# Optimization experiments

Measured on AMD Instinct MI355X. Metric: run time of the kernel, lower is better.

The kernel has to match this reference:

```python
import jax, jax.numpy as jnp
import numpy as np

N_NODES = 100000
N_EDGES = 1600000
D_IN = 128
D_OUT = 128


def setup_inputs() -> dict:
    key = jax.random.key(0)
    k_x, k_e, k_wl, k_bl, k_wr = jax.random.split(key, 5)
    x = jax.random.normal(k_x, (N_NODES, D_IN), dtype=jnp.float32)
    edge_index = jax.random.randint(k_e, (2, N_EDGES), 0, N_NODES, dtype=jnp.int64)
    # PyG Linear default init ~ kaiming-uniform-ish; plain uniform is fine for a numeric reference
    s = 1.0 / np.sqrt(D_IN)
    W_l = jax.random.uniform(k_wl, (D_OUT, D_IN), minval=-s, maxval=s, dtype=jnp.float32)
    b_l = jax.random.uniform(k_bl, (D_OUT,), minval=-s, maxval=s, dtype=jnp.float32)
    W_r = jax.random.uniform(k_wr, (D_OUT, D_IN), minval=-s, maxval=s, dtype=jnp.float32)
    return {"x": x, "edge_index": edge_index, "W_l": W_l, "b_l": b_l, "W_r": W_r}


def reference(x, edge_index, W_l, b_l, W_r):
    # SAGEConv (mean aggr): messages flow src -> dst
    src = edge_index[0]  # [E]
    dst = edge_index[1]  # [E]
    msgs = x[src]  # [E, D_IN] neighbor gather
    summed = jax.ops.segment_sum(msgs, dst, num_segments=N_NODES)  # [N, D_IN]
    deg = jax.ops.segment_sum(jnp.ones_like(dst, dtype=x.dtype), dst, num_segments=N_NODES)  # [N]
    agg = summed / jnp.maximum(deg, 1.0)[:, None]  # mean with 0 for isolated nodes
    # out = lin_l(agg) + lin_r(x); bias only on lin_l (PyG default)
    out = agg @ W_l.T + b_l + x @ W_r.T
    return out
```

## Files before the change

### kernel.cpp

```cpp
#include <hip/hip_runtime.h>

#define D_FEAT 128
#define CAP 32
#define S1CAP (1 << 16)
#define S2CAP (1 << 16)
#define LOGB 7
#define LOCB 128
#define BCAP 2560
#define CHUNK 8192
#define NBUK_MAX 1024
#define BPAD 8

typedef short bf16x8 __attribute__((ext_vector_type(8)));
typedef float f32x4 __attribute__((ext_vector_type(4)));

__device__ __forceinline__ unsigned short f2bf(float f) {
    unsigned u = __builtin_bit_cast(unsigned, f);
    u += 0x7FFF + ((u >> 16) & 1);
    return (unsigned short)(u >> 16);
}


__global__ __launch_bounds__(256) void tprep_kernel(
    const int* __restrict__ ei, int* __restrict__ flag, int* __restrict__ s1cnt,
    int* __restrict__ s2cnt, int* __restrict__ bincnt) {
    const int b = blockIdx.x;
    const int t = threadIdx.x;
    for (int i = b * 256 + t; i < NBUK_MAX * BPAD; i += 8 * 256) bincnt[i] = 0;
    if (b == 0) {
        __shared__ int nzs[4];
        int nz = 0;
        for (int i = t; i < 4096; i += 256) nz |= (ei[2 * i + 1] != 0);
        unsigned long long bal = __ballot(nz);
        if ((t & 63) == 0) nzs[t >> 6] = (bal != 0ull) ? 1 : 0;
        __syncthreads();
        if (t == 0) {
            *flag = (nzs[0] | nzs[1] | nzs[2] | nzs[3]) ? 0 : 1;
            *s1cnt = 0;
            *s2cnt = 0;
        }
    }
}

__global__ __launch_bounds__(256) void bwx_kernel(
    const int* __restrict__ ei, const int* __restrict__ flag,
    int* __restrict__ bincnt, unsigned* __restrict__ bins,
    int* __restrict__ s1cnt, int* __restrict__ spill1, int E, int N, int NBUK,
    int BINB,
    const float* __restrict__ Wl, const float* __restrict__ Wr,
    unsigned short* __restrict__ Wc,
    const float4* __restrict__ x4, uint2* __restrict__ xb2, long total4) {
    const int b = blockIdx.x;
    const int t = threadIdx.x;

    if (b < BINB) {
        __shared__ int hist[NBUK_MAX];
        __shared__ int rbase[NBUK_MAX];
        const long e0 = (long)b * CHUNK;
        const int cnt = (int)min((long)CHUNK, (long)E - e0);
        const int is64 = *flag;

        for (int i = t; i < NBUK; i += 256) hist[i] = 0;
        __syncthreads();

        for (int i = t; i < cnt; i += 256) {
            long e = e0 + i;
            int dst = is64 ? (int)((const long long*)ei)[(long)E + e] : ei[(long)E + e];
            dst = min(max(dst, 0), N - 1);
            atomicAdd(&hist[dst >> LOGB], 1);
        }
        __syncthreads();

        for (int i = t; i < NBUK; i += 256) {
            int h = hist[i];
            rbase[i] = (h > 0) ? atomicAdd(&bincnt[i * BPAD], h) : 0;
            hist[i] = 0;
        }
        __syncthreads();

        for (int i = t; i < cnt; i += 256) {
            long e = e0 + i;
            int src, dst;
            if (is64) {
                src = (int)((const long long*)ei)[e];
                dst = (int)((const long long*)ei)[(long)E + e];
            } else {
                src = ei[e];
                dst = ei[(long)E + e];
            }
            src = min(max(src, 0), N - 1);
            dst = min(max(dst, 0), N - 1);
            int bk = dst >> LOGB;
            int slot = rbase[bk] + atomicAdd(&hist[bk], 1);
            if (slot < BCAP) {
                bins[(long)bk * BCAP + slot] =
                    ((unsigned)(dst & (LOCB - 1)) << 25) | (unsigned)src;
            } else {
                int sp = atomicAdd(s1cnt, 1);
                if (sp < S1CAP) {
                    spill1[2 * sp] = src;
                    spill1[2 * sp + 1] = dst;
                }
            }
        }
    } else if (b < BINB + 128) {
        int n = b - BINB;
        float w = (t < 128) ? Wl[n * 128 + t] : Wr[n * 128 + (t - 128)];
        Wc[n * 256 + t] = f2bf(w);
    } else {
        long gid = (long)(b - BINB - 128) * 256 + t;
        if (gid < total4) {
            float4 v = x4[gid];
            uint2 o;
            o.x = (unsigned)f2bf(v.x) | ((unsigned)f2bf(v.y) << 16);
            o.y = (unsigned)f2bf(v.z) | ((unsigned)f2bf(v.w) << 16);
            xb2[gid] = o;
        }
    }
}

__global__ __launch_bounds__(256) void fill2_kernel(
    const unsigned* __restrict__ bins, const int* __restrict__ bincnt,
    int* __restrict__ adj, int* __restrict__ cursor,
    const int* __restrict__ s1cnt, const int* __restrict__ spill1,
    int* __restrict__ s2cnt, int* __restrict__ spill2, int N) {
    __shared__ int cur[LOCB];
    const int bk = blockIdx.x;
    const int t = threadIdx.x;
    if (t < LOCB) cur[t] = 0;
    __syncthreads();
    const int cnt = min(bincnt[bk * BPAD], BCAP);
    const int nb = bk << LOGB;
    for (int i = t; i < cnt; i += 256) {
        unsigned v = bins[(long)bk * BCAP + i];
        int src = (int)(v & 0x1FFFFFFu);
        int ld = (int)(v >> 25);
        int slot = atomicAdd(&cur[ld], 1);
        int dst = nb + ld;
        if (slot < CAP) {
            adj[(long)dst * CAP + slot] = src;
        } else {
            int sp = atomicAdd(s2cnt, 1);
            if (sp < S2CAP) {
                spill2[2 * sp] = src;
                spill2[2 * sp + 1] = dst;
            }
        }
    }
    const int sc = min(*s1cnt, S1CAP);
    for (int i = t; i < sc; i += 256) {
        int dst = spill1[2 * i + 1];
        if ((dst >> LOGB) == bk) {
            int src = spill1[2 * i];
            int ld = dst & (LOCB - 1);
            int slot = atomicAdd(&cur[ld], 1);
            if (slot < CAP) {
                adj[(long)dst * CAP + slot] = src;
            } else {
                int sp = atomicAdd(s2cnt, 1);
                if (sp < S2CAP) {
                    spill2[2 * sp] = src;
                    spill2[2 * sp + 1] = dst;
                }
            }
        }
    }
    __syncthreads();
    if (t < LOCB && nb + t < N) cursor[nb + t] = cur[t];
}

__device__ __forceinline__ void acc_row(float* acc, uint4 v) {
    acc[0] += __builtin_bit_cast(float, v.x << 16);
    acc[1] += __builtin_bit_cast(float, v.x & 0xFFFF0000u);
    acc[2] += __builtin_bit_cast(float, v.y << 16);
    acc[3] += __builtin_bit_cast(float, v.y & 0xFFFF0000u);
    acc[4] += __builtin_bit_cast(float, v.z << 16);
    acc[5] += __builtin_bit_cast(float, v.z & 0xFFFF0000u);
    acc[6] += __builtin_bit_cast(float, v.w << 16);
    acc[7] += __builtin_bit_cast(float, v.w & 0xFFFF0000u);
}

__device__ __forceinline__ int pick_src(int adjv, int adjv2, int e, int cq, int qd) {
    int ec = e & 31;
    int s = __shfl((ec < 16) ? adjv : adjv2, qd * 16 + (ec & 15));
    return (e < cq) ? s : 0;
}

__global__ __launch_bounds__(256) void gg_kernel(
    const unsigned int* __restrict__ xb, const int* __restrict__ cursor,
    const int* __restrict__ adj, const unsigned short* __restrict__ Wc,
    const float* __restrict__ bl, float* __restrict__ out, int N) {
    __shared__ __align__(16) unsigned short A[16 * 264];

    const int t = threadIdx.x;
    const int wv = t >> 6;
    const int lane = t & 63;
    const int n0 = blockIdx.x * 16;
    const int fq = lane & 15;
    const int qd = lane >> 4;

    const int n = n0 + wv * 4 + qd;
    const int nc = min(n, N - 1);

    const int deg = (n < N) ? cursor[n] : 0;
    int adjv = adj[(long)nc * CAP + fq];
    int adjv2 = adj[(long)nc * CAP + 16 + fq];

    unsigned xv[4];
#pragma unroll
    for (int q = 0; q < 4; ++q) {
        int nn = n0 + wv * 4 + q;
        xv[q] = (nn < N) ? xb[(long)nn * 64 + lane] : 0u;
    }

    adjv = min(max(adjv, 0), N - 1);
    adjv2 = min(max(adjv2, 0), N - 1);

    const int cq = min(deg, CAP);
    int mx = max(cq, __shfl_xor(cq, 16));
    mx = max(mx, __shfl_xor(mx, 32));
    mx = (mx + 3) & ~3;

    float acc[8] = {0.f, 0.f, 0.f, 0.f, 0.f, 0.f, 0.f, 0.f};
    uint4 va[4], vb[4];
#pragma unroll
    for (int j = 0; j < 4; ++j) {
        int s = pick_src(adjv, adjv2, j, cq, qd);
        va[j] = *(const uint4*)&xb[(long)s * 64 + fq * 4];
    }
    for (int base = 0; base < mx; base += 4) {
#pragma unroll
        for (int j = 0; j < 4; ++j) {
            int s = pick_src(adjv, adjv2, base + 4 + j, cq, qd);
            vb[j] = *(const uint4*)&xb[(long)s * 64 + fq * 4];
        }
#pragma unroll
        for (int j = 0; j < 4; ++j) {
            if (base + j < cq) acc_row(acc, va[j]);
        }
#pragma unroll
        for (int j = 0; j < 4; ++j) va[j] = vb[j];
    }

    const float iv = 1.0f / (float)max(deg, 1);
    uint4 o;
    o.x = (unsigned)f2bf(acc[0] * iv) | ((unsigned)f2bf(acc[1] * iv) << 16);
    o.y = (unsigned)f2bf(acc[2] * iv) | ((unsigned)f2bf(acc[3] * iv) << 16);
    o.z = (unsigned)f2bf(acc[4] * iv) | ((unsigned)f2bf(acc[5] * iv) << 16);
    o.w = (unsigned)f2bf(acc[6] * iv) | ((unsigned)f2bf(acc[7] * iv) << 16);
    *(uint4*)&A[(wv * 4 + qd) * 264 + fq * 8] = o;
#pragma unroll
    for (int q = 0; q < 4; ++q)
        *(unsigned*)&A[(wv * 4 + q) * 264 + 128 + 2 * lane] = xv[q];
    __syncthreads();

    const int l15 = lane & 15;
    const int quad = lane >> 4;
    f32x4 acc2[2];
    acc2[0] = (f32x4){0.f, 0.f, 0.f, 0.f};
    acc2[1] = (f32x4){0.f, 0.f, 0.f, 0.f};

#pragma unroll
    for (int kc = 0; kc < 8; ++kc) {
        const int k0 = kc * 32;
        bf16x8 af = *(const bf16x8*)&A[l15 * 264 + k0 + quad * 8];
#pragma unroll
        for (int nt = 0; nt < 2; ++nt) {
            int col = wv * 32 + nt * 16 + l15;
            bf16x8 bf = *(const bf16x8*)&Wc[col * 256 + k0 + quad * 8];
            acc2[nt] = __builtin_amdgcn_mfma_f32_16x16x32_bf16(af, bf, acc2[nt], 0, 0, 0);
        }
    }

#pragma unroll
    for (int nt = 0; nt < 2; ++nt) {
        int col = wv * 32 + nt * 16 + l15;
        float bias = bl[col];
#pragma unroll
        for (int r = 0; r < 4; ++r) {
            int node = n0 + quad * 4 + r;
            if (node < N) out[(long)node * 128 + col] = acc2[nt][r] + bias;
        }
    }
}

__global__ __launch_bounds__(256) void spill2_kernel(
    const float* __restrict__ x, const float* __restrict__ Wl,
    const int* __restrict__ cursor, const int* __restrict__ s2cnt,
    const int* __restrict__ spill2, float* __restrict__ out) {
    const int wv = threadIdx.x >> 6;
    const int lane = threadIdx.x & 63;
    const int sc = min(*s2cnt, S2CAP);
    for (int i = blockIdx.x * 4 + wv; i < sc; i += gridDim.x * 4) {
        int src = spill2[2 * i];
        int dst = spill2[2 * i + 1];
        float inv = 1.0f / (float)max(cursor[dst], 1);
#pragma unroll
        for (int cc = 0; cc < 2; ++cc) {
            int c = lane + cc * 64;
            float s = 0.0f;
            for (int k = 0; k < 128; k += 4) {
                float4 w4 = *(const float4*)&Wl[c * 128 + k];
                float4 x4 = *(const float4*)&x[(long)src * 128 + k];
                s += w4.x * x4.x + w4.y * x4.y + w4.z * x4.z + w4.w * x4.w;
            }
            atomicAdd(&out[(long)dst * 128 + c], s * inv);
        }
    }
}

extern "C" void kernel_launch(void* const* d_in, const int* in_sizes, int n_in,
                              void* d_out, int out_size, void* d_ws, size_t ws_size,
                              hipStream_t stream) {
    const float* x = (const float*)d_in[0];
    const int* ei = (const int*)d_in[1];
    const float* Wl = (const float*)d_in[2];
    const float* bl = (const float*)d_in[3];
    const float* Wr = (const float*)d_in[4];
    float* out = (float*)d_out;

    const int N = in_sizes[0] / D_FEAT;
    const int E = in_sizes[1] / 2;
    const int NBUK = (N + LOCB - 1) >> LOGB;
    const int BINB = (E + CHUNK - 1) / CHUNK;

    int* wsI = (int*)d_ws;
    int* flag = wsI;
    int* cursor = flag + 64;
    int* s1cnt = cursor + N;
    int* spill1 = s1cnt + 64;
    int* s2cnt = spill1 + 2 * S1CAP;
    int* spill2 = s2cnt + 64;
    int* bincnt = spill2 + 2 * S2CAP;
    unsigned* bins = (unsigned*)(bincnt + NBUK_MAX * BPAD);
    int* adj = (int*)(bins + (long)NBUK * BCAP);
    unsigned short* Wc = (unsigned short*)(adj + (long)N * CAP);
    unsigned int* xb = (unsigned int*)(Wc + 128 * 256);

    const long total4 = (long)N * 32;
    const int XBB = (int)((total4 + 255) / 256);

    tprep_kernel<<<8, 256, 0, stream>>>(ei, flag, s1cnt, s2cnt, bincnt);
    bwx_kernel<<<BINB + 128 + XBB, 256, 0, stream>>>(
        ei, flag, bincnt, bins, s1cnt, spill1, E, N, NBUK, BINB, Wl, Wr, Wc,
        (const float4*)x, (uint2*)xb, total4);
    fill2_kernel<<<NBUK, 256, 0, stream>>>(bins, bincnt, adj, cursor, s1cnt, spill1,
                                           s2cnt, spill2, N);
    gg_kernel<<<(N + 15) / 16, 256, 0, stream>>>(xb, cursor, adj, Wc, bl, out, N);
    spill2_kernel<<<64, 256, 0, stream>>>(x, Wl, cursor, s2cnt, spill2, out);
}
```

Before: 261.4 us.

## Fuse binning, conversion and fill into one persistent kernel with work queues

Replaces the separate binning and fill kernels with a single persistent kernel of fixed block count. Blocks claim work from atomic queues: first edge chunks, then weight and feature conversion, then a spin-wait on a done counter, then per-bucket fill. This removes a kernel launch boundary and overlaps the bf16 conversion with the binning tail. Each edge chunk is now read once and staged in shared memory instead of being read twice. The risks are the software grid barrier, which assumes all 1280 blocks are co-resident to avoid deadlock, and the lower occupancy from the larger shared-memory footprint.

```diff
diff --git a/kernel.cpp b/kernel.cpp
--- a/kernel.cpp
+++ b/kernel.cpp
@@ -7,9 +7,11 @@
 #define LOGB 7
 #define LOCB 128
 #define BCAP 2560
-#define CHUNK 8192
+#define CHUNK 4096
 #define NBUK_MAX 1024
 #define BPAD 8
+#define USPAN 8
+#define BUILD_BLOCKS 1280
 
 typedef short bf16x8 __attribute__((ext_vector_type(8)));
 typedef float f32x4 __attribute__((ext_vector_type(4)));
@@ -23,11 +25,12 @@
 
 __global__ __launch_bounds__(256) void tprep_kernel(
     const int* __restrict__ ei, int* __restrict__ flag, int* __restrict__ s1cnt,
-    int* __restrict__ s2cnt, int* __restrict__ bincnt) {
+    int* __restrict__ s2cnt, int* __restrict__ bincnt, int* __restrict__ q) {
     const int b = blockIdx.x;
     const int t = threadIdx.x;
     for (int i = b * 256 + t; i < NBUK_MAX * BPAD; i += 8 * 256) bincnt[i] = 0;
     if (b == 0) {
+        if (t < 64) q[t] = 0;
         __shared__ int nzs[4];
         int nz = 0;
         for (int i = t; i < 4096; i += 256) nz |= (ei[2 * i + 1] != 0);
@@ -42,42 +45,38 @@
     }
 }
 
-__global__ __launch_bounds__(256) void bwx_kernel(
+__global__ __launch_bounds__(256) void build_kernel(
     const int* __restrict__ ei, const int* __restrict__ flag,
     int* __restrict__ bincnt, unsigned* __restrict__ bins,
-    int* __restrict__ s1cnt, int* __restrict__ spill1, int E, int N, int NBUK,
-    int BINB,
+    int* __restrict__ s1cnt, int* __restrict__ spill1,
+    int* __restrict__ s2cnt, int* __restrict__ spill2,
+    int* __restrict__ adj, int* __restrict__ cursor,
     const float* __restrict__ Wl, const float* __restrict__ Wr,
     unsigned short* __restrict__ Wc,
-    const float4* __restrict__ x4, uint2* __restrict__ xb2, long total4) {
-    const int b = blockIdx.x;
+    const float4* __restrict__ x4, uint2* __restrict__ xb2, long total4,
+    int* __restrict__ q, int E, int N, int NBUK, int NCHUNK, int NXBU) {
+    __shared__ int hist[NBUK_MAX];
+    __shared__ int rbase[NBUK_MAX];
+    __shared__ unsigned ent[CHUNK];
+    __shared__ unsigned short ebk[CHUNK];
+    __shared__ int claim;
     const int t = threadIdx.x;
-
-    if (b < BINB) {
-        __shared__ int hist[NBUK_MAX];
-        __shared__ int rbase[NBUK_MAX];
-        const long e0 = (long)b * CHUNK;
+    const int is64 = *flag;
+    int* binq = q + 0;
+    int* xbq = q + 8;
+    int* fillq = q + 16;
+    int* done = q + 24;
+
+    for (;;) {
+        __syncthreads();
+        if (t == 0) claim = atomicAdd(binq, 1);
+        __syncthreads();
+        const int c = claim;
+        if (c >= NCHUNK) break;
+        const long e0 = (long)c * CHUNK;
         const int cnt = (int)min((long)CHUNK, (long)E - e0);
-        const int is64 = *flag;
-
         for (int i = t; i < NBUK; i += 256) hist[i] = 0;
         __syncthreads();
-
-        for (int i = t; i < cnt; i += 256) {
-            long e = e0 + i;
-            int dst = is64 ? (int)((const long long*)ei)[(long)E + e] : ei[(long)E + e];
-            dst = min(max(dst, 0), N - 1);
-            atomicAdd(&hist[dst >> LOGB], 1);
-        }
-        __syncthreads();
-
-        for (int i = t; i < NBUK; i += 256) {
-            int h = hist[i];
-            rbase[i] = (h > 0) ? atomicAdd(&bincnt[i * BPAD], h) : 0;
-            hist[i] = 0;
-        }
-        __syncthreads();
-
         for (int i = t; i < cnt; i += 256) {
             long e = e0 + i;
             int src, dst;
@@ -91,82 +90,113 @@
             src = min(max(src, 0), N - 1);
             dst = min(max(dst, 0), N - 1);
             int bk = dst >> LOGB;
+            ent[i] = ((unsigned)(dst & (LOCB - 1)) << 25) | (unsigned)src;
+            ebk[i] = (unsigned short)bk;
+            atomicAdd(&hist[bk], 1);
+        }
+        __syncthreads();
+        for (int i = t; i < NBUK; i += 256) {
+            int h = hist[i];
+            rbase[i] = (h > 0) ? atomicAdd(&bincnt[i * BPAD], h) : 0;
+            hist[i] = 0;
+        }
+        __syncthreads();
+        for (int i = t; i < cnt; i += 256) {
+            int bk = ebk[i];
             int slot = rbase[bk] + atomicAdd(&hist[bk], 1);
             if (slot < BCAP) {
-                bins[(long)bk * BCAP + slot] =
-                    ((unsigned)(dst & (LOCB - 1)) << 25) | (unsigned)src;
+                bins[(long)bk * BCAP + slot] = ent[i];
             } else {
+                unsigned v = ent[i];
                 int sp = atomicAdd(s1cnt, 1);
                 if (sp < S1CAP) {
-                    spill1[2 * sp] = src;
-                    spill1[2 * sp + 1] = dst;
+                    spill1[2 * sp] = (int)(v & 0x1FFFFFFu);
+                    spill1[2 * sp + 1] = (bk << LOGB) | (int)(v >> 25);
                 }
             }
         }
-    } else if (b < BINB + 128) {
-        int n = b - BINB;
-        float w = (t < 128) ? Wl[n * 128 + t] : Wr[n * 128 + (t - 128)];
-        Wc[n * 256 + t] = f2bf(w);
-    } else {
-        long gid = (long)(b - BINB - 128) * 256 + t;
-        if (gid < total4) {
-            float4 v = x4[gid];
-            uint2 o;
-            o.x = (unsigned)f2bf(v.x) | ((unsigned)f2bf(v.y) << 16);
-            o.y = (unsigned)f2bf(v.z) | ((unsigned)f2bf(v.w) << 16);
-            xb2[gid] = o;
-        }
-    }
-}
-
-__global__ __launch_bounds__(256) void fill2_kernel(
-    const unsigned* __restrict__ bins, const int* __restrict__ bincnt,
-    int* __restrict__ adj, int* __restrict__ cursor,
-    const int* __restrict__ s1cnt, const int* __restrict__ spill1,
-    int* __restrict__ s2cnt, int* __restrict__ spill2, int N) {
-    __shared__ int cur[LOCB];
-    const int bk = blockIdx.x;
-    const int t = threadIdx.x;
-    if (t < LOCB) cur[t] = 0;
+        __threadfence();
+        __syncthreads();
+        if (t == 0) atomicAdd(done, 1);
+    }
+
+    for (;;) {
+        __syncthreads();
+        if (t == 0) claim = atomicAdd(xbq, 1);
+        __syncthreads();
+        const int c = claim;
+        if (c >= 128 + NXBU) break;
+        if (c < 128) {
+            float w = (t < 128) ? Wl[c * 128 + t] : Wr[c * 128 + (t - 128)];
+            Wc[c * 256 + t] = f2bf(w);
+        } else {
+            long g0 = (long)(c - 128) * (256 * USPAN);
+#pragma unroll
+            for (int u = 0; u < USPAN; ++u) {
+                long gid = g0 + u * 256 + t;
+                if (gid < total4) {
+                    float4 v = x4[gid];
+                    uint2 o;
+                    o.x = (unsigned)f2bf(v.x) | ((unsigned)f2bf(v.y) << 16);
+                    o.y = (unsigned)f2bf(v.z) | ((unsigned)f2bf(v.w) << 16);
+                    xb2[gid] = o;
+                }
+            }
+        }
+    }
+
+    if (t == 0) {
+        while (atomicAdd(done, 0) < NCHUNK) __builtin_amdgcn_s_sleep(32);
+    }
     __syncthreads();
-    const int cnt = min(bincnt[bk * BPAD], BCAP);
-    const int nb = bk << LOGB;
-    for (int i = t; i < cnt; i += 256) {
-        unsigned v = bins[(long)bk * BCAP + i];
-        int src = (int)(v & 0x1FFFFFFu);
-        int ld = (int)(v >> 25);
-        int slot = atomicAdd(&cur[ld], 1);
-        int dst = nb + ld;
-        if (slot < CAP) {
-            adj[(long)dst * CAP + slot] = src;
-        } else {
-            int sp = atomicAdd(s2cnt, 1);
-            if (sp < S2CAP) {
-                spill2[2 * sp] = src;
-                spill2[2 * sp + 1] = dst;
-            }
-        }
-    }
-    const int sc = min(*s1cnt, S1CAP);
-    for (int i = t; i < sc; i += 256) {
-        int dst = spill1[2 * i + 1];
-        if ((dst >> LOGB) == bk) {
-            int src = spill1[2 * i];
-            int ld = dst & (LOCB - 1);
+    __threadfence();
+    int* cur = hist;
+    for (;;) {
+        __syncthreads();
+        if (t == 0) claim = atomicAdd(fillq, 1);
+        __syncthreads();
+        const int bk = claim;
+        if (bk >= NBUK) break;
+        if (t < LOCB) cur[t] = 0;
+        __syncthreads();
+        const int cnt = min(bincnt[bk * BPAD], BCAP);
+        const int nb = bk << LOGB;
+        for (int i = t; i < cnt; i += 256) {
+            unsigned v = bins[(long)bk * BCAP + i];
+            int src = (int)(v & 0x1FFFFFFu);
+            int ld = (int)(v >> 25);
             int slot = atomicAdd(&cur[ld], 1);
             if (slot < CAP) {
-                adj[(long)dst * CAP + slot] = src;
+                adj[(long)(nb + ld) * CAP + slot] = src;
             } else {
                 int sp = atomicAdd(s2cnt, 1);
                 if (sp < S2CAP) {
                     spill2[2 * sp] = src;
-                    spill2[2 * sp + 1] = dst;
+                    spill2[2 * sp + 1] = nb + ld;
                 }
             }
         }
-    }
-    __syncthreads();
-    if (t < LOCB && nb + t < N) cursor[nb + t] = cur[t];
+        const int sc = min(*s1cnt, S1CAP);
+        for (int i = t; i < sc; i += 256) {
+            int dst = spill1[2 * i + 1];
+            if ((dst >> LOGB) == bk) {
+                int src = spill1[2 * i];
+                int ld = dst & (LOCB - 1);
+                int slot = atomicAdd(&cur[ld], 1);
+                if (slot < CAP) {
+                    adj[(long)dst * CAP + slot] = src;
+                } else {
+                    int sp = atomicAdd(s2cnt, 1);
+                    if (sp < S2CAP) {
+                        spill2[2 * sp] = src;
+                        spill2[2 * sp + 1] = dst;
+                    }
+                }
+            }
+        }
+        __syncthreads();
+        if (t < LOCB && nb + t < N) cursor[nb + t] = cur[t];
+    }
 }
 
 __device__ __forceinline__ void acc_row(float* acc, uint4 v) {
@@ -322,7 +352,7 @@
     const int N = in_sizes[0] / D_FEAT;
     const int E = in_sizes[1] / 2;
     const int NBUK = (N + LOCB - 1) >> LOGB;
-    const int BINB = (E + CHUNK - 1) / CHUNK;
+    const int NCHUNK = (E + CHUNK - 1) / CHUNK;
 
     int* wsI = (int*)d_ws;
     int* flag = wsI;
@@ -332,20 +362,20 @@
     int* s2cnt = spill1 + 2 * S1CAP;
     int* spill2 = s2cnt + 64;
     int* bincnt = spill2 + 2 * S2CAP;
-    unsigned* bins = (unsigned*)(bincnt + NBUK_MAX * BPAD);
+    int* q = bincnt + NBUK_MAX * BPAD;
+    unsigned* bins = (unsigned*)(q + 64);
     int* adj = (int*)(bins + (long)NBUK * BCAP);
     unsigned short* Wc = (unsigned short*)(adj + (long)N * CAP);
     unsigned int* xb = (unsigned int*)(Wc + 128 * 256);
 
     const long total4 = (long)N * 32;
-    const int XBB = (int)((total4 + 255) / 256);
-
-    tprep_kernel<<<8, 256, 0, stream>>>(ei, flag, s1cnt, s2cnt, bincnt);
-    bwx_kernel<<<BINB + 128 + XBB, 256, 0, stream>>>(
-        ei, flag, bincnt, bins, s1cnt, spill1, E, N, NBUK, BINB, Wl, Wr, Wc,
-        (const float4*)x, (uint2*)xb, total4);
-    fill2_kernel<<<NBUK, 256, 0, stream>>>(bins, bincnt, adj, cursor, s1cnt, spill1,
-                                           s2cnt, spill2, N);
+    const int NXBU = (int)((total4 + 256 * USPAN - 1) / (256 * USPAN));
+
+    tprep_kernel<<<8, 256, 0, stream>>>(ei, flag, s1cnt, s2cnt, bincnt, q);
+    build_kernel<<<BUILD_BLOCKS, 256, 0, stream>>>(
+        ei, flag, bincnt, bins, s1cnt, spill1, s2cnt, spill2, adj, cursor,
+        Wl, Wr, Wc, (const float4*)x, (uint2*)xb, total4, q, E, N, NBUK,
+        NCHUNK, NXBU);
     gg_kernel<<<(N + 15) / 16, 256, 0, stream>>>(xb, cursor, adj, Wc, bl, out, N);
     spill2_kernel<<<64, 256, 0, stream>>>(x, Wl, cursor, s2cnt, spill2, out);
 }
```

New measurement: 551.3 us. +110.9%, slower.

## Stage edge entries in LDS for single global read; build adjacency tiles in shared memory

Applied to the files above, without the earlier changes.

The binning kernel now reads each edge's src/dst once, packs the entry and bucket id into shared memory and builds the histogram in the same pass. The second pass scatters from LDS instead of re-reading the edge index from global memory, and CHUNK is halved so the staging arrays fit in LDS. The fill kernel assembles each bucket's adjacency rows in a shared-memory image and writes them to global memory with coalesced 16-byte stores instead of scattered 4-byte stores. The trade-off is higher LDS use per block, which may lower occupancy, plus twice as many binning blocks and therefore more global atomics on the bin counters.

```diff
diff --git a/kernel.cpp b/kernel.cpp
--- a/kernel.cpp
+++ b/kernel.cpp
@@ -7,7 +7,7 @@
 #define LOGB 7
 #define LOCB 128
 #define BCAP 2560
-#define CHUNK 8192
+#define CHUNK 4096
 #define NBUK_MAX 1024
 #define BPAD 8
 
@@ -56,26 +56,13 @@
     if (b < BINB) {
         __shared__ int hist[NBUK_MAX];
         __shared__ int rbase[NBUK_MAX];
+        __shared__ unsigned ent[CHUNK];
+        __shared__ unsigned short ebk[CHUNK];
         const long e0 = (long)b * CHUNK;
         const int cnt = (int)min((long)CHUNK, (long)E - e0);
         const int is64 = *flag;
 
         for (int i = t; i < NBUK; i += 256) hist[i] = 0;
-        __syncthreads();
-
-        for (int i = t; i < cnt; i += 256) {
-            long e = e0 + i;
-            int dst = is64 ? (int)((const long long*)ei)[(long)E + e] : ei[(long)E + e];
-            dst = min(max(dst, 0), N - 1);
-            atomicAdd(&hist[dst >> LOGB], 1);
-        }
-        __syncthreads();
-
-        for (int i = t; i < NBUK; i += 256) {
-            int h = hist[i];
-            rbase[i] = (h > 0) ? atomicAdd(&bincnt[i * BPAD], h) : 0;
-            hist[i] = 0;
-        }
         __syncthreads();
 
         for (int i = t; i < cnt; i += 256) {
@@ -91,15 +78,30 @@
             src = min(max(src, 0), N - 1);
             dst = min(max(dst, 0), N - 1);
             int bk = dst >> LOGB;
+            ent[i] = ((unsigned)(dst & (LOCB - 1)) << 25) | (unsigned)src;
+            ebk[i] = (unsigned short)bk;
+            atomicAdd(&hist[bk], 1);
+        }
+        __syncthreads();
+
+        for (int i = t; i < NBUK; i += 256) {
+            int h = hist[i];
+            rbase[i] = (h > 0) ? atomicAdd(&bincnt[i * BPAD], h) : 0;
+            hist[i] = 0;
+        }
+        __syncthreads();
+
+        for (int i = t; i < cnt; i += 256) {
+            int bk = ebk[i];
             int slot = rbase[bk] + atomicAdd(&hist[bk], 1);
             if (slot < BCAP) {
-                bins[(long)bk * BCAP + slot] =
-                    ((unsigned)(dst & (LOCB - 1)) << 25) | (unsigned)src;
+                bins[(long)bk * BCAP + slot] = ent[i];
             } else {
+                unsigned v = ent[i];
                 int sp = atomicAdd(s1cnt, 1);
                 if (sp < S1CAP) {
-                    spill1[2 * sp] = src;
-                    spill1[2 * sp + 1] = dst;
+                    spill1[2 * sp] = (int)(v & 0x1FFFFFFu);
+                    spill1[2 * sp + 1] = (bk << LOGB) | (int)(v >> 25);
                 }
             }
         }
@@ -125,6 +127,7 @@
     const int* __restrict__ s1cnt, const int* __restrict__ spill1,
     int* __restrict__ s2cnt, int* __restrict__ spill2, int N) {
     __shared__ int cur[LOCB];
+    __shared__ __align__(16) int adjimg[LOCB * CAP];
     const int bk = blockIdx.x;
     const int t = threadIdx.x;
     if (t < LOCB) cur[t] = 0;
@@ -136,14 +139,13 @@
         int src = (int)(v & 0x1FFFFFFu);
         int ld = (int)(v >> 25);
         int slot = atomicAdd(&cur[ld], 1);
-        int dst = nb + ld;
         if (slot < CAP) {
-            adj[(long)dst * CAP + slot] = src;
+            adjimg[ld * CAP + slot] = src;
         } else {
             int sp = atomicAdd(s2cnt, 1);
             if (sp < S2CAP) {
                 spill2[2 * sp] = src;
-                spill2[2 * sp + 1] = dst;
+                spill2[2 * sp + 1] = nb + ld;
             }
         }
     }
@@ -155,7 +157,7 @@
             int ld = dst & (LOCB - 1);
             int slot = atomicAdd(&cur[ld], 1);
             if (slot < CAP) {
-                adj[(long)dst * CAP + slot] = src;
+                adjimg[ld * CAP + slot] = src;
             } else {
                 int sp = atomicAdd(s2cnt, 1);
                 if (sp < S2CAP) {
@@ -166,6 +168,11 @@
         }
     }
     __syncthreads();
+    const int lim = min(LOCB, N - nb);
+    const int nvec = lim * CAP / 4;
+    uint4* dstp = (uint4*)&adj[(long)nb * CAP];
+    const uint4* srcp = (const uint4*)adjimg;
+    for (int i = t; i < nvec; i += 256) dstp[i] = srcp[i];
     if (t < LOCB && nb + t < N) cursor[nb + t] = cur[t];
 }
 
```

Measured after the change: 243.9 us. -6.7%, faster.
